# Performance work log

Hardware: AMD Instinct MI355X
Metric: run time of the kernel (lower is better)

The kernel has to match this reference:

```python
import jax, jax.numpy as jnp
import numpy as np

B, N, E, H = 4, 2048, 1024, 16
D = E // H
SCALE = 1.0 / np.sqrt(D).astype(np.float32)


def setup_inputs() -> dict:
    key = jax.random.key(0)
    ks = jax.random.split(key, 8)
    xq = jax.random.normal(ks[0], (B, N, E), jnp.float32)
    xk = jax.random.normal(ks[1], (B, N, E), jnp.float32)
    xv = jax.random.normal(ks[2], (B, N, E), jnp.float32)
    # causal mask: True means 'masked out' (matches masked_fill_ semantics)
    attn_mask = jnp.triu(jnp.ones((N, N), dtype=bool), k=1)[None, None]
    Wq = jax.random.normal(ks[3], (E, E), jnp.float32) / np.sqrt(E)
    Wk = jax.random.normal(ks[4], (E, E), jnp.float32) / np.sqrt(E)
    Wv = jax.random.normal(ks[5], (E, E), jnp.float32) / np.sqrt(E)
    Wo = jax.random.normal(ks[6], (E, E), jnp.float32) / np.sqrt(E)
    bo = jnp.zeros((E,), jnp.float32)
    return {"xq": xq, "xk": xk, "xv": xv, "attn_mask": attn_mask,
            "Wq": Wq, "Wk": Wk, "Wv": Wv, "Wo": Wo, "bo": bo}


def _split_heads(x):
    # [B, N, E] -> [B, H, N, D]
    return x.reshape(B, N, H, D).transpose(0, 2, 1, 3)


def reference(xq, xk, xv, attn_mask, Wq, Wk, Wv, Wo, bo):
    # torch nn.Linear: y = x @ W.T
    q = _split_heads(xq @ Wq.T)
    k = _split_heads(xk @ Wk.T)
    v = _split_heads(xv @ Wv.T)
    scores = SCALE * jnp.einsum('bhqd,bhkd->bhqk', q, k)
    scores = jnp.where(attn_mask, -jnp.inf, scores)
    attn = jax.nn.softmax(scores, axis=-1)
    out = jnp.einsum('bhqk,bhkd->bhqd', attn, v)
    out = out.transpose(0, 2, 1, 3).reshape(B, N, E)  # merge heads
    return out @ Wo.T + bo
```

## Files before the change

kernel.cpp:

```cpp
#include <hip/hip_runtime.h>
#include <hip/hip_bf16.h>
#include <stdint.h>
#include <stddef.h>

#define B_ 4
#define N_ 2048
#define E_ 1024
#define H_ 16
#define D_ 64

using bf16 = __hip_bfloat16;
typedef __bf16 bf16x8 __attribute__((ext_vector_type(8)));
typedef float  f32x4  __attribute__((ext_vector_type(4)));
typedef float  f32x16 __attribute__((ext_vector_type(16)));
typedef unsigned int u32x2 __attribute__((ext_vector_type(2)));

__device__ inline bf16x8 load8(const float* p) {
    f32x4 a = *(const f32x4*)p;
    f32x4 b = *(const f32x4*)(p + 4);
    bf16x8 r;
#pragma unroll
    for (int e = 0; e < 4; e++) { r[e] = (__bf16)a[e]; r[e + 4] = (__bf16)b[e]; }
    return r;
}
__device__ inline void store_elem(float* C, size_t idx, float v) { C[idx] = v; }
__device__ inline void store_elem(bf16* C, size_t idx, float v) {
    C[idx] = __float2bfloat16(v);
}

__device__ inline void async_stage16(const bf16* g, bf16* l) {
    __builtin_amdgcn_global_load_lds(
        (const __attribute__((address_space(1))) uint32_t*)g,
        (__attribute__((address_space(3))) uint32_t*)l, 16, 0, 0);
}
__device__ inline void manual_stage16(const float* g, bf16* l) {
    *(bf16x8*)l = load8(g);
}

__global__ __launch_bounds__(256) void cvt_all(
    const float* __restrict__ w0, const float* __restrict__ w1,
    const float* __restrict__ w2, const float* __restrict__ w3,
    bf16* __restrict__ wd,
    const float* __restrict__ x0, const float* __restrict__ x1,
    const float* __restrict__ x2,
    bf16* __restrict__ xd0, bf16* __restrict__ xd1, bf16* __restrict__ xd2)
{
    int bx = blockIdx.x;
    const float* s; bf16* d;
    if (bx < 2048) {
        const int seg = bx >> 9;
        s = seg == 0 ? w0 : seg == 1 ? w1 : seg == 2 ? w2 : w3;
        d = wd + (size_t)seg * (E_ * E_);
        bx &= 511;
    } else {
        bx -= 2048;
        const int seg = bx >> 12;
        s = seg == 0 ? x0 : seg == 1 ? x1 : x2;
        d = seg == 0 ? xd0 : seg == 1 ? xd1 : xd2;
        bx &= 4095;
    }
    const size_t off = ((size_t)bx * 256 + threadIdx.x) * 8;
    *(bf16x8*)&d[off] = load8(s + off);
}

struct GemmB { const void* A[3]; void* C[3]; };

template <typename TA, typename TC>
__global__ __launch_bounds__(256) void gemm_bt(
    GemmB batch, const bf16* __restrict__ Wb, const float* __restrict__ bias)
{
    __shared__ bf16 As[128 * 32];
    __shared__ bf16 Bs[128 * 32];

    const TA*   __restrict__ A = (const TA*)batch.A[blockIdx.z];
    TC*         __restrict__ C = (TC*)batch.C[blockIdx.z];
    const bf16* __restrict__ W = Wb + (size_t)blockIdx.z * (E_ * E_);

    const int tid  = threadIdx.x;
    const int lane = tid & 63;
    const int wave = tid >> 6;
    const int wr   = wave >> 1;
    const int wc   = wave & 1;
    const int r    = lane & 15;
    const int quad = lane >> 4;

    const int m0 = blockIdx.y * 128;
    const int n0 = blockIdx.x * 128;

    const int row0 = tid >> 2,         cc0 = (tid & 3) * 8;
    const int row1 = (tid + 256) >> 2, cc1 = cc0;

    f32x4 acc[4][4];
#pragma unroll
    for (int i = 0; i < 4; i++)
#pragma unroll
        for (int j = 0; j < 4; j++)
            acc[i][j] = {0.0f, 0.0f, 0.0f, 0.0f};

    for (int k0 = 0; k0 < E_; k0 += 32) {
        __syncthreads();
        if constexpr (__is_same(TA, bf16)) {
            async_stage16(&A[(size_t)(m0 + row0) * E_ + k0 + cc0], &As[tid * 8]);
            async_stage16(&A[(size_t)(m0 + row1) * E_ + k0 + cc1], &As[(tid + 256) * 8]);
        } else {
            manual_stage16(&A[(size_t)(m0 + row0) * E_ + k0 + cc0], &As[tid * 8]);
            manual_stage16(&A[(size_t)(m0 + row1) * E_ + k0 + cc1], &As[(tid + 256) * 8]);
        }
        async_stage16(&W[(size_t)(n0 + row0) * E_ + k0 + cc0], &Bs[tid * 8]);
        async_stage16(&W[(size_t)(n0 + row1) * E_ + k0 + cc1], &Bs[(tid + 256) * 8]);
        __syncthreads();

        bf16x8 a[4], b[4];
#pragma unroll
        for (int mt = 0; mt < 4; mt++)
            a[mt] = *(const bf16x8*)&As[(wr * 64 + mt * 16 + r) * 32 + quad * 8];
#pragma unroll
        for (int nt = 0; nt < 4; nt++)
            b[nt] = *(const bf16x8*)&Bs[(wc * 64 + nt * 16 + r) * 32 + quad * 8];
#pragma unroll
        for (int mt = 0; mt < 4; mt++)
#pragma unroll
            for (int nt = 0; nt < 4; nt++)
                acc[mt][nt] = __builtin_amdgcn_mfma_f32_16x16x32_bf16(
                    a[mt], b[nt], acc[mt][nt], 0, 0, 0);
    }

#pragma unroll
    for (int mt = 0; mt < 4; mt++) {
#pragma unroll
        for (int nt = 0; nt < 4; nt++) {
            const int col = n0 + wc * 64 + nt * 16 + r;
            float bv = bias ? bias[col] : 0.0f;
#pragma unroll
            for (int rg = 0; rg < 4; rg++) {
                const int row = m0 + wr * 64 + mt * 16 + quad * 4 + rg;
                store_elem(C, (size_t)row * E_ + col, acc[mt][nt][rg] + bv);
            }
        }
    }
}

__global__ __launch_bounds__(256) void attn_fwd(
    const bf16* __restrict__ q, const bf16* __restrict__ k,
    const bf16* __restrict__ v, bf16* __restrict__ o)
{
    constexpr int LS = 72;
    constexpr float LOG2E = 1.44269504088896340736f;
    __shared__ bf16 Ks[2][64 * LS];
    __shared__ bf16 Vt[2][64 * LS];

    const int tid  = threadIdx.x;
    const int lane = tid & 63;
    const int wave = tid >> 6;
    const int l31  = lane & 31;
    const int hi   = lane >> 5;

    const int bh = blockIdx.y;
    const int b  = bh >> 4;
    const int h  = bh & 15;
    const int p  = blockIdx.x;

    const size_t basek = (size_t)b * N_ * E_ + (size_t)h * D_;

    const int key0 = tid >> 3;
    const int key1 = key0 + 32;
    const int ck   = (tid & 7) * 8;
    const int kp   = tid & 31;
    const int cv   = (tid >> 5) * 8;

#pragma unroll
    for (int ph = 0; ph < 2; ph++) {
        const int xb = ph == 0 ? (15 - p) : p;
        const int q0 = xb * 128;
        const int nt = 2 * xb + 2;

        bf16x8 qB[4];
        {
            const size_t qoff =
                ((size_t)b * N_ + q0 + wave * 32 + l31) * E_ + h * D_ + hi * 8;
#pragma unroll
            for (int kc = 0; kc < 4; kc++) {
                qB[kc] = *(const bf16x8*)&q[qoff + kc * 16];
#pragma unroll
                for (int e = 0; e < 8; e++)
                    qB[kc][e] = (__bf16)((float)qB[kc][e] * 0.125f);
            }
        }

        float m_i = -1e30f;
        float l_i = 0.0f;
        f32x16 o_acc[2];
#pragma unroll
        for (int rg = 0; rg < 16; rg++) { o_acc[0][rg] = 0.0f; o_acc[1][rg] = 0.0f; }

        bf16x8 kp0, kp1, vp0, vp1;
        kp0 = *(const bf16x8*)&k[basek + (size_t)key0 * E_ + ck];
        kp1 = *(const bf16x8*)&k[basek + (size_t)key1 * E_ + ck];
        vp0 = *(const bf16x8*)&v[basek + (size_t)(2 * kp) * E_ + cv];
        vp1 = *(const bf16x8*)&v[basek + (size_t)(2 * kp + 1) * E_ + cv];
        *(bf16x8*)&Ks[0][key0 * LS + ck] = kp0;
        *(bf16x8*)&Ks[0][key1 * LS + ck] = kp1;
#pragma unroll
        for (int e = 0; e < 8; e++) {
            union { __bf16 hh[2]; uint32_t u; } pk;
            pk.hh[0] = vp0[e]; pk.hh[1] = vp1[e];
            *(uint32_t*)&Vt[0][(cv + e) * LS + 2 * kp] = pk.u;
        }
        {
            const size_t j1 = 64;
            kp0 = *(const bf16x8*)&k[basek + (j1 + key0) * E_ + ck];
            kp1 = *(const bf16x8*)&k[basek + (j1 + key1) * E_ + ck];
            vp0 = *(const bf16x8*)&v[basek + (j1 + 2 * kp) * E_ + cv];
            vp1 = *(const bf16x8*)&v[basek + (j1 + 2 * kp + 1) * E_ + cv];
        }
        __syncthreads();

        for (int t = 0; t < nt; t++) {
            const int cur = t & 1;

            if (t + 1 < nt) {
                *(bf16x8*)&Ks[cur ^ 1][key0 * LS + ck] = kp0;
                *(bf16x8*)&Ks[cur ^ 1][key1 * LS + ck] = kp1;
#pragma unroll
                for (int e = 0; e < 8; e++) {
                    union { __bf16 hh[2]; uint32_t u; } pk;
                    pk.hh[0] = vp0[e]; pk.hh[1] = vp1[e];
                    *(uint32_t*)&Vt[cur ^ 1][(cv + e) * LS + 2 * kp] = pk.u;
                }
            }
            if (t + 2 < nt) {
                const size_t j2 = (size_t)(t + 2) * 64;
                kp0 = *(const bf16x8*)&k[basek + (j2 + key0) * E_ + ck];
                kp1 = *(const bf16x8*)&k[basek + (j2 + key1) * E_ + ck];
                vp0 = *(const bf16x8*)&v[basek + (j2 + 2 * kp) * E_ + cv];
                vp1 = *(const bf16x8*)&v[basek + (j2 + 2 * kp + 1) * E_ + cv];
            }

            f32x16 sf[2];
#pragma unroll
            for (int rg = 0; rg < 16; rg++) { sf[0][rg] = 0.0f; sf[1][rg] = 0.0f; }
#pragma unroll
            for (int kc = 0; kc < 4; kc++) {
                bf16x8 ka0 = *(const bf16x8*)&Ks[cur][l31 * LS + kc * 16 + hi * 8];
                bf16x8 ka1 = *(const bf16x8*)&Ks[cur][(32 + l31) * LS + kc * 16 + hi * 8];
                sf[0] = __builtin_amdgcn_mfma_f32_32x32x16_bf16(ka0, qB[kc], sf[0], 0, 0, 0);
                sf[1] = __builtin_amdgcn_mfma_f32_32x32x16_bf16(ka1, qB[kc], sf[1], 0, 0, 0);
            }

            if (t >= nt - 2) {
                const int qgl   = q0 + wave * 32 + l31;
                const int kbase = t * 64 + 4 * hi;
#pragma unroll
                for (int mt = 0; mt < 2; mt++)
#pragma unroll
                    for (int rg = 0; rg < 16; rg++) {
                        const int kgl = kbase + mt * 32 + (rg & 3) + 8 * (rg >> 2);
                        if (kgl > qgl) sf[mt][rg] = -1e30f;
                    }
            }

            float mhalf[8];
#pragma unroll
            for (int i = 0; i < 8; i++)
                mhalf[i] = fmaxf(fmaxf(sf[0][2 * i], sf[0][2 * i + 1]),
                                 fmaxf(sf[1][2 * i], sf[1][2 * i + 1]));
            float mx = fmaxf(fmaxf(fmaxf(mhalf[0], mhalf[1]), fmaxf(mhalf[2], mhalf[3])),
                             fmaxf(fmaxf(mhalf[4], mhalf[5]), fmaxf(mhalf[6], mhalf[7])));
            mx = fmaxf(mx, __shfl_xor(mx, 32));

            if (!__all(mx <= m_i + 8.0f)) {
                const float m_new = fmaxf(m_i, mx);
                const float al = exp2f((m_i - m_new) * LOG2E);
                l_i *= al;
#pragma unroll
                for (int mo = 0; mo < 2; mo++)
#pragma unroll
                    for (int rg = 0; rg < 16; rg++) o_acc[mo][rg] *= al;
                m_i = m_new;
            }

            const float m2 = m_i * LOG2E;
#pragma unroll
            for (int mt = 0; mt < 2; mt++)
#pragma unroll
                for (int rg = 0; rg < 16; rg++)
                    sf[mt][rg] = exp2f(__builtin_fmaf(sf[mt][rg], LOG2E, -m2));

            float ls = 0.0f;
#pragma unroll
            for (int mt = 0; mt < 2; mt++) {
                const float a0 = (sf[mt][0] + sf[mt][1]) + (sf[mt][2] + sf[mt][3]);
                const float a1 = (sf[mt][4] + sf[mt][5]) + (sf[mt][6] + sf[mt][7]);
                const float a2 = (sf[mt][8] + sf[mt][9]) + (sf[mt][10] + sf[mt][11]);
                const float a3 = (sf[mt][12] + sf[mt][13]) + (sf[mt][14] + sf[mt][15]);
                ls += (a0 + a1) + (a2 + a3);
            }
            ls += __shfl_xor(ls, 32);
            l_i += ls;

            uint32_t w[2][8];
#pragma unroll
            for (int mt = 0; mt < 2; mt++)
#pragma unroll
                for (int i = 0; i < 8; i++) {
                    union { __bf16 hh[2]; uint32_t u; } pk;
                    pk.hh[0] = (__bf16)sf[mt][2 * i];
                    pk.hh[1] = (__bf16)sf[mt][2 * i + 1];
                    w[mt][i] = pk.u;
                }

#pragma unroll
            for (int ks = 0; ks < 4; ks++) {
                const int c  = 4 * (ks & 1);
                const int mt = ks >> 1;
                u32x2 r1 = __builtin_amdgcn_permlane32_swap(
                    w[mt][c + 0], w[mt][c + 2], false, false);
                u32x2 r2 = __builtin_amdgcn_permlane32_swap(
                    w[mt][c + 1], w[mt][c + 3], false, false);
                union { uint32_t u[4]; bf16x8 v8; } pbu;
                pbu.u[0] = r1[0]; pbu.u[1] = r2[0];
                pbu.u[2] = r1[1]; pbu.u[3] = r2[1];
#pragma unroll
                for (int mo = 0; mo < 2; mo++) {
                    bf16x8 va = *(const bf16x8*)
                        &Vt[cur][(mo * 32 + l31) * LS + ks * 16 + hi * 8];
                    o_acc[mo] = __builtin_amdgcn_mfma_f32_32x32x16_bf16(
                        va, pbu.v8, o_acc[mo], 0, 0, 0);
                }
            }

            __syncthreads();
        }

        {
            const float invl = 1.0f / l_i;
            const size_t orow =
                ((size_t)b * N_ + q0 + wave * 32 + l31) * E_ + h * D_;
#pragma unroll
            for (int mo = 0; mo < 2; mo++)
#pragma unroll
                for (int g = 0; g < 4; g++) {
                    union { __bf16 hh[4]; uint2 u2; } pk;
#pragma unroll
                    for (int j = 0; j < 4; j++)
                        pk.hh[j] = (__bf16)(o_acc[mo][4 * g + j] * invl);
                    *(uint2*)&o[orow + mo * 32 + 8 * g + 4 * hi] = pk.u2;
                }
        }
    }
}

extern "C" void kernel_launch(void* const* d_in, const int* in_sizes, int n_in,
                              void* d_out, int out_size, void* d_ws, size_t ws_size,
                              hipStream_t stream) {
    const float* xq = (const float*)d_in[0];
    const float* xk = (const float*)d_in[1];
    const float* xv = (const float*)d_in[2];
    const float* Wq = (const float*)d_in[4];
    const float* Wk = (const float*)d_in[5];
    const float* Wv = (const float*)d_in[6];
    const float* Wo = (const float*)d_in[7];
    const float* bo = (const float*)d_in[8];
    float* out = (float*)d_out;

    const size_t elems = (size_t)B_ * N_ * E_;
    const size_t wel   = (size_t)E_ * E_;
    bf16* q   = (bf16*)d_ws;
    bf16* kk  = q + elems;
    bf16* vv  = kk + elems;
    bf16* ao  = vv + elems;
    bf16* Wb  = ao + elems;
    bf16* xb0 = Wb + 4 * wel;
    bf16* xb1 = xb0 + elems;
    bf16* xb2 = xb1 + elems;

    const size_t need_big = (7 * elems + 4 * wel) * 2;
    const bool big = ws_size >= need_big;

    dim3 blk(256);
    if (big) {
        cvt_all<<<dim3(14336), blk, 0, stream>>>(
            Wq, Wk, Wv, Wo, Wb, xq, xk, xv, xb0, xb1, xb2);
    } else {
        cvt_all<<<dim3(2048), blk, 0, stream>>>(
            Wq, Wk, Wv, Wo, Wb, nullptr, nullptr, nullptr,
            nullptr, nullptr, nullptr);
    }

    GemmB proj;
    if (big) { proj.A[0] = xb0; proj.A[1] = xb1; proj.A[2] = xb2; }
    else     { proj.A[0] = xq;  proj.A[1] = xk;  proj.A[2] = xv;  }
    proj.C[0] = q; proj.C[1] = kk; proj.C[2] = vv;
    if (big)
        gemm_bt<bf16, bf16><<<dim3(E_ / 128, (B_ * N_) / 128, 3), blk, 0, stream>>>(
            proj, Wb, nullptr);
    else
        gemm_bt<float, bf16><<<dim3(E_ / 128, (B_ * N_) / 128, 3), blk, 0, stream>>>(
            proj, Wb, nullptr);

    attn_fwd<<<dim3(8, B_ * H_), blk, 0, stream>>>(q, kk, vv, ao);

    GemmB fin;
    fin.A[0] = ao; fin.A[1] = ao; fin.A[2] = ao;
    fin.C[0] = out; fin.C[1] = out; fin.C[2] = out;
    gemm_bt<bf16, float><<<dim3(E_ / 128, (B_ * N_) / 128, 1), blk, 0, stream>>>(
        fin, Wb + 3 * wel, bo);
}
```

Before: 353.9 us.

## Deepen K/V register prefetch to two tiles ahead and use LDS-only barrier

Raises the register prefetch of K/V tiles in the causal attention kernel from one tile to two tiles ahead, using two register sets that alternate with the LDS double buffer. It also swaps __syncthreads for a barrier that waits only on lgkmcnt, so outstanding global loads need not drain at each tile boundary. The aim is to hide global memory latency behind more MFMA work, at the cost of extra VGPRs, which could lower occupancy.

```diff
diff --git a/kernel.cpp b/kernel.cpp
--- a/kernel.cpp
+++ b/kernel.cpp
@@ -35,6 +35,11 @@
 }
 __device__ inline void manual_stage16(const float* g, bf16* l) {
     *(bf16x8*)l = load8(g);
+}
+
+__device__ inline void lds_barrier() {
+    asm volatile("s_waitcnt lgkmcnt(0)" ::: "memory");
+    __builtin_amdgcn_s_barrier();
 }
 
 __global__ __launch_bounds__(256) void cvt_all(
@@ -168,6 +173,25 @@
     const int kp   = tid & 31;
     const int cv   = (tid >> 5) * 8;
 
+    auto LOADSET = [&](bf16x8& a0, bf16x8& a1, bf16x8& a2, bf16x8& a3, int j) {
+        const size_t jb = (size_t)j * 64;
+        a0 = *(const bf16x8*)&k[basek + (jb + key0) * E_ + ck];
+        a1 = *(const bf16x8*)&k[basek + (jb + key1) * E_ + ck];
+        a2 = *(const bf16x8*)&v[basek + (jb + 2 * kp) * E_ + cv];
+        a3 = *(const bf16x8*)&v[basek + (jb + 2 * kp + 1) * E_ + cv];
+    };
+    auto COMMIT = [&](const bf16x8& a0, const bf16x8& a1,
+                      const bf16x8& a2, const bf16x8& a3, int buf) {
+        *(bf16x8*)&Ks[buf][key0 * LS + ck] = a0;
+        *(bf16x8*)&Ks[buf][key1 * LS + ck] = a1;
+#pragma unroll
+        for (int e = 0; e < 8; e++) {
+            union { __bf16 hh[2]; uint32_t u; } pk;
+            pk.hh[0] = a2[e]; pk.hh[1] = a3[e];
+            *(uint32_t*)&Vt[buf][(cv + e) * LS + 2 * kp] = pk.u;
+        }
+    };
+
 #pragma unroll
     for (int ph = 0; ph < 2; ph++) {
         const int xb = ph == 0 ? (15 - p) : p;
@@ -193,47 +217,23 @@
 #pragma unroll
         for (int rg = 0; rg < 16; rg++) { o_acc[0][rg] = 0.0f; o_acc[1][rg] = 0.0f; }
 
-        bf16x8 kp0, kp1, vp0, vp1;
-        kp0 = *(const bf16x8*)&k[basek + (size_t)key0 * E_ + ck];
-        kp1 = *(const bf16x8*)&k[basek + (size_t)key1 * E_ + ck];
-        vp0 = *(const bf16x8*)&v[basek + (size_t)(2 * kp) * E_ + cv];
-        vp1 = *(const bf16x8*)&v[basek + (size_t)(2 * kp + 1) * E_ + cv];
-        *(bf16x8*)&Ks[0][key0 * LS + ck] = kp0;
-        *(bf16x8*)&Ks[0][key1 * LS + ck] = kp1;
-#pragma unroll
-        for (int e = 0; e < 8; e++) {
-            union { __bf16 hh[2]; uint32_t u; } pk;
-            pk.hh[0] = vp0[e]; pk.hh[1] = vp1[e];
-            *(uint32_t*)&Vt[0][(cv + e) * LS + 2 * kp] = pk.u;
-        }
-        {
-            const size_t j1 = 64;
-            kp0 = *(const bf16x8*)&k[basek + (j1 + key0) * E_ + ck];
-            kp1 = *(const bf16x8*)&k[basek + (j1 + key1) * E_ + ck];
-            vp0 = *(const bf16x8*)&v[basek + (j1 + 2 * kp) * E_ + cv];
-            vp1 = *(const bf16x8*)&v[basek + (j1 + 2 * kp + 1) * E_ + cv];
-        }
-        __syncthreads();
+        bf16x8 s0k0, s0k1, s0v0, s0v1;
+        bf16x8 s1k0, s1k1, s1v0, s1v1;
+        LOADSET(s0k0, s0k1, s0v0, s0v1, 0);
+        COMMIT(s0k0, s0k1, s0v0, s0v1, 0);
+        LOADSET(s1k0, s1k1, s1v0, s1v1, 1);
+        if (2 < nt) LOADSET(s0k0, s0k1, s0v0, s0v1, 2);
+        lds_barrier();
 
         for (int t = 0; t < nt; t++) {
             const int cur = t & 1;
 
-            if (t + 1 < nt) {
-                *(bf16x8*)&Ks[cur ^ 1][key0 * LS + ck] = kp0;
-                *(bf16x8*)&Ks[cur ^ 1][key1 * LS + ck] = kp1;
-#pragma unroll
-                for (int e = 0; e < 8; e++) {
-                    union { __bf16 hh[2]; uint32_t u; } pk;
-                    pk.hh[0] = vp0[e]; pk.hh[1] = vp1[e];
-                    *(uint32_t*)&Vt[cur ^ 1][(cv + e) * LS + 2 * kp] = pk.u;
-                }
-            }
-            if (t + 2 < nt) {
-                const size_t j2 = (size_t)(t + 2) * 64;
-                kp0 = *(const bf16x8*)&k[basek + (j2 + key0) * E_ + ck];
-                kp1 = *(const bf16x8*)&k[basek + (j2 + key1) * E_ + ck];
-                vp0 = *(const bf16x8*)&v[basek + (j2 + 2 * kp) * E_ + cv];
-                vp1 = *(const bf16x8*)&v[basek + (j2 + 2 * kp + 1) * E_ + cv];
+            if (cur == 0) {
+                if (t + 1 < nt) COMMIT(s1k0, s1k1, s1v0, s1v1, 1);
+                if (t + 3 < nt) LOADSET(s1k0, s1k1, s1v0, s1v1, t + 3);
+            } else {
+                if (t + 1 < nt) COMMIT(s0k0, s0k1, s0v0, s0v1, 0);
+                if (t + 3 < nt) LOADSET(s0k0, s0k1, s0v0, s0v1, t + 3);
             }
 
             f32x16 sf[2];
@@ -329,7 +329,7 @@
                 }
             }
 
-            __syncthreads();
+            lds_barrier();
         }
 
         {
```

Measured after the change: 364.9 us. 1.03x slower.
